# Performance work log

Measured on AMD Instinct MI355X. Metric: run time of the kernel, lower is better.

The kernel has to match this reference:

```python
import jax, jax.numpy as jnp
import numpy as np

STD_SEP2 = 0.05 ** 2  # 0.0025
COEF = -0.001 / STD_SEP2  # -0.4


def setup_inputs() -> dict:
    key = jax.random.key(0)
    keypoints = jax.random.uniform(key, (64, 8192, 2), dtype=jnp.float32)
    return {"keypoints": keypoints}


def reference(keypoints):
    B, N, C = keypoints.shape
    # Original computes, for each pair (i, j), i != j:
    #   d_ij = sqrt( sum over batch AND coords of (K[:,i,:] - K[:,j,:])**2 )
    #   loss += exp(-0.001 * d_ij / std_sep^2)
    # i.e. a Frobenius norm over the full [B, C] slice per keypoint pair.
    # Flatten each keypoint's [B, C] slice into a row vector -> [N, B*C],
    # then use the ||a||^2 + ||b||^2 - 2 a.b trick for all pairwise distances.
    X = jnp.transpose(keypoints, (1, 0, 2)).reshape(N, B * C)  # [N, B*C]
    sq = jnp.sum(X * X, axis=1)                                # [N]
    d2 = sq[:, None] + sq[None, :] - 2.0 * (X @ X.T)           # [N, N]
    eye = jnp.eye(N, dtype=bool)
    # guard diagonal / tiny negatives before sqrt (exact zeros would NaN grads)
    d2_safe = jnp.maximum(jnp.where(eye, 1.0, d2), 0.0)
    d = jnp.sqrt(d2_safe)
    loss = jnp.sum(jnp.where(eye, 0.0, jnp.exp(COEF * d)))
    return loss
```

## Files before the change

kernel.cpp:

```cpp
#include <hip/hip_runtime.h>
#include <hip/hip_bf16.h>


#define N_KP   8192
#define KDIM   128
#define NT     64
#define NTILES (NT * (NT + 1) / 2)
#define COEF2  (-0.57707801635558535f)

typedef __attribute__((ext_vector_type(8))) short bf16x8;
typedef __attribute__((ext_vector_type(4))) float f32x4;


__device__ __forceinline__ unsigned short f2bf(float f) {
    unsigned int u = __builtin_bit_cast(unsigned int, f);
    unsigned int r = (u + 0x7FFFu + ((u >> 16) & 1u)) >> 16;
    return (unsigned short)r;
}

__device__ __forceinline__ float bf2f(unsigned short u) {
    unsigned int x = ((unsigned int)u) << 16;
    return __builtin_bit_cast(float, x);
}

__device__ __forceinline__ void gload_lds16(const void* g, void* l) {
    __builtin_amdgcn_global_load_lds(
        (const __attribute__((address_space(1))) unsigned int*)g,
        (__attribute__((address_space(3))) unsigned int*)l, 16, 0, 0);
}

__global__ __launch_bounds__(256) void prep_kernel(
        const float* __restrict__ in, unsigned short* __restrict__ Xbf,
        float* __restrict__ sq) {
    int tid = threadIdx.x;
    int p = tid >> 5, idx = tid & 31;
    int n = blockIdx.x * 32 + idx;
    int t16 = n >> 4, l16 = n & 15;
    unsigned int* dst = (unsigned int*)Xbf;
    float s = 0.0f;
    #pragma unroll
    for (int q = 0; q < 8; ++q) {
        int b = p * 8 + q;
        float2 v = *(const float2*)(in + (size_t)b * (N_KP * 2) + n * 2);
        unsigned short h0 = f2bf(v.x);
        unsigned short h1 = f2bf(v.y);
        float f0 = bf2f(h0), f1 = bf2f(h1);
        s = fmaf(f0, f0, s);
        s = fmaf(f1, f1, s);
        unsigned int off_us = (((unsigned)(t16 * 4 + (b >> 4)) * 64
                                + ((b >> 2) & 3) * 16 + l16) << 3) + ((b & 3) << 1);
        dst[off_us >> 1] = ((unsigned int)h1 << 16) | h0;
    }
    __shared__ float wsq[256];
    wsq[tid] = s;
    __syncthreads();
    if (tid < 32) {
        float t = 0.0f;
        #pragma unroll
        for (int pp = 0; pp < 8; ++pp) t += wsq[pp * 32 + tid];
        sq[blockIdx.x * 32 + tid] = t;
    }
}

__global__ __launch_bounds__(256) void pair_kernel(
        const unsigned short* __restrict__ Xbf, const float* __restrict__ sq,
        float* __restrict__ partials) {
    int bid = blockIdx.x;
    int ti = (int)((129.0f - sqrtf(129.0f * 129.0f - 8.0f * (float)bid)) * 0.5f);
    while (ti > 0 && ti * (129 - ti) / 2 > bid) --ti;
    while ((ti + 1) * (129 - (ti + 1)) / 2 <= bid) ++ti;
    int tj = ti + (bid - ti * (129 - ti) / 2);

    int wid  = threadIdx.x >> 6;
    int lane = threadIdx.x & 63;
    int wr = wid >> 1, wc = wid & 1;
    int l16 = lane & 15, lhi = lane >> 4;

    __shared__ __align__(16) unsigned short tileLDS[64 * 512];

    const char* src_base = (const char*)Xbf;
    #pragma unroll
    for (int c0 = 0; c0 < 16; ++c0) {
        int c = wid * 16 + c0;
        int fidx = (c < 32) ? (ti * 32 + c) : (tj * 32 + (c - 32));
        gload_lds16(src_base + (size_t)fidx * 1024 + lane * 16,
                    (char*)tileLDS + (size_t)c * 1024);
    }
    __syncthreads();

    const bf16x8* L = (const bf16x8*)tileLDS;
    int abase = (wr * 4) * 4;
    int bbase = (8 + wc * 4) * 4;

    f32x4 acc[4][4] = {};
    #pragma unroll
    for (int kk = 0; kk < 4; ++kk) {
        bf16x8 a[4], b[4];
        #pragma unroll
        for (int m = 0; m < 4; ++m)
            a[m] = L[(abase + m * 4 + kk) * 64 + lane];
        #pragma unroll
        for (int n = 0; n < 4; ++n)
            b[n] = L[(bbase + n * 4 + kk) * 64 + lane];
        #pragma unroll
        for (int m = 0; m < 4; ++m)
            #pragma unroll
            for (int n = 0; n < 4; ++n)
                acc[m][n] = __builtin_amdgcn_mfma_f32_16x16x32_bf16(
                    a[m], b[n], acc[m][n], 0, 0, 0);
    }

    int ibase = ti * 128 + wr * 64;
    int jbase = tj * 128 + wc * 64;

    float si[4][4];
    #pragma unroll
    for (int m = 0; m < 4; ++m)
        #pragma unroll
        for (int r = 0; r < 4; ++r)
            si[m][r] = sq[ibase + m * 16 + lhi * 4 + r];
    float sqj[4];
    #pragma unroll
    for (int n = 0; n < 4; ++n) sqj[n] = sq[jbase + n * 16 + l16];

    float p[4] = {0.0f, 0.0f, 0.0f, 0.0f};
    #pragma unroll
    for (int m = 0; m < 4; ++m) {
        #pragma unroll
        for (int n = 0; n < 4; ++n) {
            #pragma unroll
            for (int r = 0; r < 4; ++r) {
                float d2 = fmaf(-2.0f, acc[m][n][r], si[m][r] + sqj[n]);
                float d = __builtin_amdgcn_sqrtf(fabsf(d2));
                p[r] += __builtin_amdgcn_exp2f(COEF2 * d);
            }
        }
    }
    float partial = (p[0] + p[1]) + (p[2] + p[3]);

    #pragma unroll
    for (int m = 32; m; m >>= 1) partial += __shfl_xor(partial, m, 64);
    __shared__ float wsum[4];
    if (lane == 0) wsum[wid] = partial;
    __syncthreads();
    if (threadIdx.x == 0) {
        float v = (wsum[0] + wsum[1]) + (wsum[2] + wsum[3]);
        if (ti == tj) v -= 128.0f; else v *= 2.0f;
        partials[bid] = v;
    }
}

__global__ __launch_bounds__(256) void reduce_kernel(
        const float* __restrict__ partials, float* __restrict__ out) {
    float s = 0.0f;
    for (int i = threadIdx.x; i < NTILES; i += 256) s += partials[i];
    #pragma unroll
    for (int m = 32; m; m >>= 1) s += __shfl_xor(s, m, 64);
    __shared__ float wsum[4];
    int wid = threadIdx.x >> 6, lane = threadIdx.x & 63;
    if (lane == 0) wsum[wid] = s;
    __syncthreads();
    if (threadIdx.x == 0) out[0] = (wsum[0] + wsum[1]) + (wsum[2] + wsum[3]);
}

extern "C" void kernel_launch(void* const* d_in, const int* in_sizes, int n_in,
                              void* d_out, int out_size, void* d_ws, size_t ws_size,
                              hipStream_t stream) {
    const float* in = (const float*)d_in[0];
    float* out = (float*)d_out;

    unsigned short* Xbf = (unsigned short*)d_ws;
    float* sq = (float*)((char*)d_ws + (size_t)N_KP * KDIM * 2);
    float* partials = (float*)((char*)d_ws + (size_t)N_KP * KDIM * 2
                               + (size_t)N_KP * 4);

    prep_kernel<<<N_KP / 32, 256, 0, stream>>>(in, Xbf, sq);
    pair_kernel<<<NTILES, 256, 0, stream>>>(Xbf, sq, partials);
    reduce_kernel<<<1, 256, 0, stream>>>(partials, out);
}
```

Measured before the change: 34.68 us.

## Make pair kernel persistent with double-buffered B tiles and register-resident A

Replaces one-block-per-tile launch with 512 persistent blocks that each walk a contiguous range of upper-triangular tiles. The A operand and its squared norms stay in registers and reload only when the row tile changes, and the B tile is double-buffered in LDS so the next tile's global load overlaps current MFMA and exp work. This cuts per-block launch/setup and A-tile reloads, at the cost of more registers (64 bf16x8 A values), a barrier every step, and possible load imbalance between blocks.

```diff
diff --git a/kernel.cpp b/kernel.cpp
--- a/kernel.cpp
+++ b/kernel.cpp
@@ -6,6 +6,7 @@
 #define KDIM   128
 #define NT     64
 #define NTILES (NT * (NT + 1) / 2)
+#define NBLK   512
 #define COEF2  (-0.57707801635558535f)
 
 typedef __attribute__((ext_vector_type(8))) short bf16x8;
@@ -66,94 +67,142 @@
         const unsigned short* __restrict__ Xbf, const float* __restrict__ sq,
         float* __restrict__ partials) {
     int bid = blockIdx.x;
-    int ti = (int)((129.0f - sqrtf(129.0f * 129.0f - 8.0f * (float)bid)) * 0.5f);
-    while (ti > 0 && ti * (129 - ti) / 2 > bid) --ti;
-    while ((ti + 1) * (129 - (ti + 1)) / 2 <= bid) ++ti;
-    int tj = ti + (bid - ti * (129 - ti) / 2);
+    int start = (bid * NTILES) >> 9;
+    int end   = ((bid + 1) * NTILES) >> 9;
+    int nsteps = end - start;
+
+    int ti = (int)((129.0f - sqrtf(129.0f * 129.0f - 8.0f * (float)start)) * 0.5f);
+    while (ti > 0 && ti * (129 - ti) / 2 > start) --ti;
+    while ((ti + 1) * (129 - (ti + 1)) / 2 <= start) ++ti;
+    int tj = ti + (start - ti * (129 - ti) / 2);
 
     int wid  = threadIdx.x >> 6;
     int lane = threadIdx.x & 63;
     int wr = wid >> 1, wc = wid & 1;
     int l16 = lane & 15, lhi = lane >> 4;
 
-    __shared__ __align__(16) unsigned short tileLDS[64 * 512];
-
-    const char* src_base = (const char*)Xbf;
-    #pragma unroll
-    for (int c0 = 0; c0 < 16; ++c0) {
-        int c = wid * 16 + c0;
-        int fidx = (c < 32) ? (ti * 32 + c) : (tj * 32 + (c - 32));
-        gload_lds16(src_base + (size_t)fidx * 1024 + lane * 16,
-                    (char*)tileLDS + (size_t)c * 1024);
-    }
-    __syncthreads();
-
-    const bf16x8* L = (const bf16x8*)tileLDS;
-    int abase = (wr * 4) * 4;
-    int bbase = (8 + wc * 4) * 4;
-
-    f32x4 acc[4][4] = {};
-    #pragma unroll
-    for (int kk = 0; kk < 4; ++kk) {
-        bf16x8 a[4], b[4];
+    __shared__ __align__(16) unsigned short B_lds[2][32 * 512];
+    __shared__ float wsum[4];
+
+    const bf16x8* Xs8 = (const bf16x8*)Xbf;
+
+    bf16x8 a[4][4];
+    float si[4][4];
+    {
         #pragma unroll
         for (int m = 0; m < 4; ++m)
-            a[m] = L[(abase + m * 4 + kk) * 64 + lane];
-        #pragma unroll
-        for (int n = 0; n < 4; ++n)
-            b[n] = L[(bbase + n * 4 + kk) * 64 + lane];
+            #pragma unroll
+            for (int kk = 0; kk < 4; ++kk)
+                a[m][kk] = Xs8[(size_t)((ti * 8 + wr * 4 + m) * 4 + kk) * 64 + lane];
         #pragma unroll
         for (int m = 0; m < 4; ++m)
             #pragma unroll
+            for (int r = 0; r < 4; ++r)
+                si[m][r] = sq[ti * 128 + wr * 64 + m * 16 + lhi * 4 + r];
+    }
+
+    #pragma unroll
+    for (int c0 = 0; c0 < 8; ++c0) {
+        int c = wid * 8 + c0;
+        gload_lds16((const char*)Xbf + ((size_t)(tj * 32 + c)) * 1024 + lane * 16,
+                    (char*)B_lds[0] + (size_t)c * 1024);
+    }
+    __syncthreads();
+
+    float run = 0.0f;
+    int ndiag = 0;
+    int cur = 0;
+    int cti = ti, ctj = tj;
+
+    for (int t = 0; t < nsteps; ++t) {
+        int nti = cti, ntj = ctj + 1;
+        if (ntj == NT) { ++nti; ntj = nti; }
+
+        if (t + 1 < nsteps) {
+            #pragma unroll
+            for (int c0 = 0; c0 < 8; ++c0) {
+                int c = wid * 8 + c0;
+                gload_lds16((const char*)Xbf + ((size_t)(ntj * 32 + c)) * 1024 + lane * 16,
+                            (char*)B_lds[cur ^ 1] + (size_t)c * 1024);
+            }
+        }
+
+        float sqj[4];
+        #pragma unroll
+        for (int n = 0; n < 4; ++n) sqj[n] = sq[ctj * 128 + wc * 64 + n * 16 + l16];
+
+        const bf16x8* L = (const bf16x8*)B_lds[cur];
+        f32x4 acc[4][4] = {};
+        #pragma unroll
+        for (int kk = 0; kk < 4; ++kk) {
+            bf16x8 b[4];
+            #pragma unroll
             for (int n = 0; n < 4; ++n)
-                acc[m][n] = __builtin_amdgcn_mfma_f32_16x16x32_bf16(
-                    a[m], b[n], acc[m][n], 0, 0, 0);
-    }
-
-    int ibase = ti * 128 + wr * 64;
-    int jbase = tj * 128 + wc * 64;
-
-    float si[4][4];
-    #pragma unroll
-    for (int m = 0; m < 4; ++m)
-        #pragma unroll
-        for (int r = 0; r < 4; ++r)
-            si[m][r] = sq[ibase + m * 16 + lhi * 4 + r];
-    float sqj[4];
-    #pragma unroll
-    for (int n = 0; n < 4; ++n) sqj[n] = sq[jbase + n * 16 + l16];
-
-    float p[4] = {0.0f, 0.0f, 0.0f, 0.0f};
-    #pragma unroll
-    for (int m = 0; m < 4; ++m) {
-        #pragma unroll
-        for (int n = 0; n < 4; ++n) {
-            #pragma unroll
-            for (int r = 0; r < 4; ++r) {
-                float d2 = fmaf(-2.0f, acc[m][n][r], si[m][r] + sqj[n]);
-                float d = __builtin_amdgcn_sqrtf(fabsf(d2));
-                p[r] += __builtin_amdgcn_exp2f(COEF2 * d);
+                b[n] = L[((wc * 4 + n) * 4 + kk) * 64 + lane];
+            #pragma unroll
+            for (int m = 0; m < 4; ++m)
+                #pragma unroll
+                for (int n = 0; n < 4; ++n)
+                    acc[m][n] = __builtin_amdgcn_mfma_f32_16x16x32_bf16(
+                        a[m][kk], b[n], acc[m][n], 0, 0, 0);
+        }
+
+        float p0 = 0.0f, p1 = 0.0f, p2 = 0.0f, p3 = 0.0f;
+        #pragma unroll
+        for (int m = 0; m < 4; ++m) {
+            #pragma unroll
+            for (int n = 0; n < 4; ++n) {
+                float base0 = si[m][0] + sqj[n];
+                float base1 = si[m][1] + sqj[n];
+                float base2 = si[m][2] + sqj[n];
+                float base3 = si[m][3] + sqj[n];
+                float d2_0 = fmaf(-2.0f, acc[m][n][0], base0);
+                float d2_1 = fmaf(-2.0f, acc[m][n][1], base1);
+                float d2_2 = fmaf(-2.0f, acc[m][n][2], base2);
+                float d2_3 = fmaf(-2.0f, acc[m][n][3], base3);
+                p0 += __builtin_amdgcn_exp2f(COEF2 * __builtin_amdgcn_sqrtf(fabsf(d2_0)));
+                p1 += __builtin_amdgcn_exp2f(COEF2 * __builtin_amdgcn_sqrtf(fabsf(d2_1)));
+                p2 += __builtin_amdgcn_exp2f(COEF2 * __builtin_amdgcn_sqrtf(fabsf(d2_2)));
+                p3 += __builtin_amdgcn_exp2f(COEF2 * __builtin_amdgcn_sqrtf(fabsf(d2_3)));
             }
         }
-    }
-    float partial = (p[0] + p[1]) + (p[2] + p[3]);
-
-    #pragma unroll
-    for (int m = 32; m; m >>= 1) partial += __shfl_xor(partial, m, 64);
-    __shared__ float wsum[4];
-    if (lane == 0) wsum[wid] = partial;
+        float s = (p0 + p1) + (p2 + p3);
+        bool diag = (cti == ctj);
+        run += diag ? s : 2.0f * s;
+        ndiag += diag ? 1 : 0;
+
+        if (t + 1 < nsteps && nti != cti) {
+            #pragma unroll
+            for (int m = 0; m < 4; ++m)
+                #pragma unroll
+                for (int kk = 0; kk < 4; ++kk)
+                    a[m][kk] = Xs8[(size_t)((nti * 8 + wr * 4 + m) * 4 + kk) * 64 + lane];
+            #pragma unroll
+            for (int m = 0; m < 4; ++m)
+                #pragma unroll
+                for (int r = 0; r < 4; ++r)
+                    si[m][r] = sq[nti * 128 + wr * 64 + m * 16 + lhi * 4 + r];
+        }
+
+        __syncthreads();
+        cur ^= 1;
+        cti = nti; ctj = ntj;
+    }
+
+    #pragma unroll
+    for (int m = 32; m; m >>= 1) run += __shfl_xor(run, m, 64);
+    if (lane == 0) wsum[wid] = run;
     __syncthreads();
     if (threadIdx.x == 0) {
         float v = (wsum[0] + wsum[1]) + (wsum[2] + wsum[3]);
-        if (ti == tj) v -= 128.0f; else v *= 2.0f;
-        partials[bid] = v;
+        partials[bid] = v - 128.0f * (float)ndiag;
     }
 }
 
 __global__ __launch_bounds__(256) void reduce_kernel(
         const float* __restrict__ partials, float* __restrict__ out) {
     float s = 0.0f;
-    for (int i = threadIdx.x; i < NTILES; i += 256) s += partials[i];
+    for (int i = threadIdx.x; i < NBLK; i += 256) s += partials[i];
     #pragma unroll
     for (int m = 32; m; m >>= 1) s += __shfl_xor(s, m, 64);
     __shared__ float wsum[4];
@@ -175,6 +224,6 @@
                                + (size_t)N_KP * 4);
 
     prep_kernel<<<N_KP / 32, 256, 0, stream>>>(in, Xbf, sq);
-    pair_kernel<<<NTILES, 256, 0, stream>>>(Xbf, sq, partials);
+    pair_kernel<<<NBLK, 256, 0, stream>>>(Xbf, sq, partials);
     reduce_kernel<<<1, 256, 0, stream>>>(partials, out);
 }
```

New measurement: 37.59 us. 1.08x slower.
